# Kernel tuning notes

Hardware: AMD Instinct MI355X
Metric: run time of the kernel (lower is better)

Reference implementation:

```python
import jax, jax.numpy as jnp
import numpy as np

# Dimensions: D must equal C_CHUNK**2 (original code's view+transpose requires it)
D = 4096        # flattened input dim per sample
C_CHUNK = 64    # chunk_size (rows of G per chunk)
N_CHUNKS = D // C_CHUNK  # = 64
H = 512         # hidden dim of forward_func MLP
C_OUT = 8       # output classes of forward_func
B = 8           # batch size (state_batch has 2*B rows)
EPS_G = 1e-4    # metric regularizer (constant under grad)


def setup_inputs() -> dict:
    key = jax.random.key(0)
    ks = jax.random.split(key, 6)
    t = jax.random.uniform(ks[0], (1,), dtype=jnp.float32)
    state_batch = jax.random.normal(ks[1], (2 * B, D), dtype=jnp.float32)
    x0_batch = jax.random.normal(ks[2], (B, D), dtype=jnp.float32)
    x1_batch = jax.random.normal(ks[3], (B, D), dtype=jnp.float32)
    W1 = jax.random.normal(ks[4], (D, H), dtype=jnp.float32) / np.float32(np.sqrt(D))
    W2 = jax.random.normal(ks[5], (H, C_OUT), dtype=jnp.float32) / np.float32(np.sqrt(H))
    return {"t": t, "state_batch": state_batch, "x0_batch": x0_batch,
            "x1_batch": x1_batch, "W1": W1, "W2": W2}


def _accel_per_sample(x, v, W1, W2):
    """Chunked Christoffel-symbol contraction for one sample.
    x: [D] current point, v: [D] deviation velocity. Returns a: [D]."""
    def f(xi):  # forward_func: 2-layer tanh MLP, [D] -> [C_OUT]
        return jnp.tanh(xi @ W1) @ W2

    ones = jnp.ones((D,), x.dtype)

    def chunk_sums(xi):
        # G = J^T J + eps*I; row_sums[i] = sum_j G[i,j] computed without
        # materializing the D x D metric: J^T (J @ 1)  (+ const eps on diag).
        J = jax.jacrev(f)(xi)              # [C_OUT, D]
        row = J.T @ (J @ ones)             # [D]
        return row.reshape(N_CHUNKS, C_CHUNK).sum(axis=1)  # [N_CHUNKS]

    g = jax.jacrev(chunk_sums)(x)          # [N_CHUNKS, D] = dG_chunk_sum/dx
    g = g.reshape(N_CHUNKS, C_CHUNK, C_CHUNK)
    g = g / (jnp.linalg.norm(g, axis=2, keepdims=True) + 1e-6)
    Gamma = 0.5 * (g + jnp.swapaxes(g, 1, 2))   # symmetrized [nc, c, c]
    vc = v.reshape(N_CHUNKS, C_CHUNK)
    # a_chunk[i] = -sum_k Gamma[i,k] v_i v_k  (Christoffel quadratic in v)
    a = -jnp.einsum('nik,ni,nk->ni', Gamma, vc, vc)
    return a.reshape(D)


def reference(t, state_batch, x0_batch, x1_batch, W1, W2):
    ts = t[0]
    Bn = state_batch.shape[0] // 2
    deviation = state_batch[:Bn]
    dev_velocity = state_batch[Bn:]
    window = 4.0 * ts * (1.0 - ts)
    x = x0_batch + ts * (x1_batch - x0_batch) + window * deviation  # [B, D]
    a = jax.vmap(_accel_per_sample, in_axes=(0, 0, None, None))(x, dev_velocity, W1, W2)
    a = a / (jnp.linalg.norm(dev_velocity, axis=1, keepdims=True) + 1e-6)
    restoration = -0.1 * deviation
    return jnp.concatenate([dev_velocity, a + restoration], axis=0)  # [2B, D]
```

## Files before the change

### kernel.cpp

```cpp
#include <hip/hip_runtime.h>

#define D 4096
#define H 512
#define NCH 64
#define CCH 64
#define B 8
#define COUT 8

typedef __bf16 bf16x8 __attribute__((ext_vector_type(8)));
typedef float  f32x4  __attribute__((ext_vector_type(4)));

#define OFF_P    0
#define OFF_UP   (OFF_P + NCH*H)
#define OFF_S    (OFF_UP + NCH*B*H)
#define OFF_ST2  (OFF_S + B*H)
#define OFF_Q    (OFF_ST2 + B*H)
#define OFF_C    (OFF_Q + B*H)
#define OFF_VN   (OFF_C + H)
#define OFF_A1   (OFF_VN + 64)
#define OFF_ZB   (OFF_A1 + B*NCH*CCH)
#define OFF_W1H  (OFF_ZB + B*64*4096)
#define OFF_W1L  (OFF_W1H + (D*H)/2)
#define OFF_WH   (OFF_W1L + (D*H)/2)
#define OFF_WL   (OFF_WH + (B*NCH*H)/2)

__device__ __forceinline__ unsigned short f2bf(float x) {
    unsigned int u = __float_as_uint(x);
    unsigned int r = (u + 0x7FFFu + ((u >> 16) & 1u)) >> 16;
    return (unsigned short)r;
}
__device__ __forceinline__ float bf2f(unsigned short s) {
    return __uint_as_float(((unsigned int)s) << 16);
}

__global__ void k1_reduce_w1(const float* __restrict__ W1,
                             const float* __restrict__ state,
                             const float* __restrict__ x0,
                             const float* __restrict__ x1,
                             const float* __restrict__ tptr,
                             float* __restrict__ ws) {
    int n   = blockIdx.x;
    int ht  = blockIdx.y;
    int tid = threadIdx.x;
    int h   = ht * 128 + tid;

    __shared__ float xs[B][64];
    float ts = tptr[0];
    float window = 4.f * ts * (1.f - ts);
    if (tid < 64) {
        int d = n * 64 + tid;
        for (int b = 0; b < B; ++b) {
            float a0 = x0[b * D + d];
            float a1v = x1[b * D + d];
            float dev = state[b * D + d];
            xs[b][tid] = a0 + ts * (a1v - a0) + window * dev;
        }
    }
    __syncthreads();

    unsigned short* __restrict__ W1Hp = (unsigned short*)(ws + OFF_W1H);
    unsigned short* __restrict__ W1Lp = (unsigned short*)(ws + OFF_W1L);

    float p = 0.f;
    float up[B];
#pragma unroll
    for (int b = 0; b < B; ++b) up[b] = 0.f;
    for (int j = 0; j < 64; ++j) {
        int d = n * 64 + j;
        float wv = W1[(size_t)d * H + h];
        unsigned short hi = f2bf(wv);
        W1Hp[d * H + h] = hi;
        W1Lp[d * H + h] = f2bf(wv - bf2f(hi));
        p += wv;
#pragma unroll
        for (int b = 0; b < B; ++b) up[b] += wv * xs[b][j];
    }
    ws[OFF_P + n * H + h] = p;
    for (int b = 0; b < B; ++b) ws[OFF_UP + (n * B + b) * H + h] = up[b];
}

__global__ void k2_sample(const float* __restrict__ W2,
                          const float* __restrict__ state,
                          float* __restrict__ ws) {
    int b = blockIdx.x, tid = threadIdx.x;
    int wid = tid >> 6, lane = tid & 63;
    __shared__ float lm[8][8];
    __shared__ float ms[8];
    __shared__ float lv[8];

    int h = tid;
    float u = 0.f, c = 0.f;
    for (int n = 0; n < NCH; ++n) {
        u += ws[OFF_UP + (n * B + b) * H + h];
        c += ws[OFF_P + n * H + h];
    }
    float tt  = tanhf(u);
    float s   = 1.f - tt * tt;
    float st2 = -2.f * tt * s;
    ws[OFF_S   + b * H + h] = s;
    ws[OFF_ST2 + b * H + h] = st2;
    ws[OFF_C   + h] = c;

    const float4* w2p = (const float4*)(W2 + h * 8);
    float4 w2a = w2p[0], w2b = w2p[1];
    float w2r[8] = {w2a.x, w2a.y, w2a.z, w2a.w, w2b.x, w2b.y, w2b.z, w2b.w};

    float cs = c * s;
    float pr[8];
#pragma unroll
    for (int o = 0; o < 8; ++o) pr[o] = cs * w2r[o];
#pragma unroll
    for (int mk = 1; mk < 64; mk <<= 1)
#pragma unroll
        for (int o = 0; o < 8; ++o) pr[o] += __shfl_xor(pr[o], mk);
    if (lane == 0)
#pragma unroll
        for (int o = 0; o < 8; ++o) lm[wid][o] = pr[o];

    float v2 = 0.f;
    const float* v = state + (size_t)(B + b) * D;
    for (int j = 0; j < D / H; ++j) { float vv = v[j * H + h]; v2 += vv * vv; }
#pragma unroll
    for (int mk = 1; mk < 64; mk <<= 1) v2 += __shfl_xor(v2, mk);
    if (lane == 0) lv[wid] = v2;
    __syncthreads();

    if (tid < 8) {
        float a = 0.f;
        for (int w = 0; w < 8; ++w) a += lm[w][tid];
        ms[tid] = a;
    }
    if (tid == 0) {
        float a = 0.f;
        for (int w = 0; w < 8; ++w) a += lv[w];
        ws[OFF_VN + b] = sqrtf(a) + 1e-6f;
    }
    __syncthreads();

    float q = 0.f;
#pragma unroll
    for (int o = 0; o < 8; ++o) q += w2r[o] * ms[o];
    ws[OFF_Q + b * H + h] = q;
}

__global__ void k3_w(const float* __restrict__ W2,
                     float* __restrict__ ws) {
    int n = blockIdx.x, b = blockIdx.y, lane = threadIdx.x;
    float M[8];
#pragma unroll
    for (int o = 0; o < 8; ++o) M[o] = 0.f;
    for (int j = 0; j < 8; ++j) {
        int h = j * 64 + lane;
        float ps = ws[OFF_P + n * H + h] * ws[OFF_S + b * H + h];
        const float4* wp = (const float4*)(W2 + h * 8);
        float4 wa = wp[0], wb = wp[1];
        M[0] += ps * wa.x; M[1] += ps * wa.y; M[2] += ps * wa.z; M[3] += ps * wa.w;
        M[4] += ps * wb.x; M[5] += ps * wb.y; M[6] += ps * wb.z; M[7] += ps * wb.w;
    }
#pragma unroll
    for (int mk = 1; mk < 64; mk <<= 1)
#pragma unroll
        for (int o = 0; o < 8; ++o) M[o] += __shfl_xor(M[o], mk);

    unsigned short* __restrict__ WHp = (unsigned short*)(ws + OFF_WH);
    unsigned short* __restrict__ WLp = (unsigned short*)(ws + OFF_WL);
    for (int j = 0; j < 8; ++j) {
        int h = j * 64 + lane;
        const float4* wp = (const float4*)(W2 + h * 8);
        float4 wa = wp[0], wb = wp[1];
        float r = wa.x*M[0] + wa.y*M[1] + wa.z*M[2] + wa.w*M[3]
                + wb.x*M[4] + wb.y*M[5] + wb.z*M[6] + wb.w*M[7];
        float P = ws[OFF_P + n * H + h];
        float wv = ws[OFF_ST2 + b * H + h] * (P * ws[OFF_Q + b * H + h] + ws[OFF_C + h] * r);
        unsigned short hi = f2bf(wv);
        WHp[(b * NCH + n) * H + h] = hi;
        WLp[(b * NCH + n) * H + h] = f2bf(wv - bf2f(hi));
    }
}

__global__ __launch_bounds__(256) void k4_mfma(const float* __restrict__ state,
                                               float* __restrict__ ws) {
    int i   = blockIdx.x;
    int b   = blockIdx.y;
    int tid = threadIdx.x;
    int wid = tid >> 6, lane = tid & 63;
    int r16 = lane & 15;
    int kgrp = (lane >> 4) * 8;

    __shared__ float vsp[64][65];
    __shared__ float gp[2][64][67];
    __shared__ float coefs[64];

    const float* v = state + (size_t)(B + b) * D;
    for (int r = 0; r < 4; ++r) {
        int fidx = tid + r * 256;
        float4 val = ((const float4*)v)[fidx];
        int base = fidx * 4, row = base >> 6, col = base & 63;
        vsp[row][col] = val.x; vsp[row][col+1] = val.y;
        vsp[row][col+2] = val.z; vsp[row][col+3] = val.w;
    }

    const unsigned short* __restrict__ W1Hp = (const unsigned short*)(ws + OFF_W1H);
    const unsigned short* __restrict__ W1Lp = (const unsigned short*)(ws + OFF_W1L);
    const unsigned short* __restrict__ WHp  = (const unsigned short*)(ws + OFF_WH);
    const unsigned short* __restrict__ WLp  = (const unsigned short*)(ws + OFF_WL);

    f32x4 acc[4][4];
    f32x4 z4 = {0.f, 0.f, 0.f, 0.f};
#pragma unroll
    for (int m = 0; m < 4; ++m)
#pragma unroll
        for (int c = 0; c < 4; ++c) acc[m][c] = z4;

    int kb = wid * 128 + kgrp;
#pragma unroll
    for (int ks = 0; ks < 4; ++ks) {
        int k = kb + ks * 32;
        bf16x8 ah[4], al[4], bh[4], bl[4];
#pragma unroll
        for (int m = 0; m < 4; ++m) {
            int off = (b * 64 + m * 16 + r16) * H + k;
            ah[m] = *(const bf16x8*)(WHp + off);
            al[m] = *(const bf16x8*)(WLp + off);
        }
#pragma unroll
        for (int c = 0; c < 4; ++c) {
            int off = (i * 64 + c * 16 + r16) * H + k;
            bh[c] = *(const bf16x8*)(W1Hp + off);
            bl[c] = *(const bf16x8*)(W1Lp + off);
        }
#pragma unroll
        for (int m = 0; m < 4; ++m)
#pragma unroll
            for (int c = 0; c < 4; ++c) {
                acc[m][c] = __builtin_amdgcn_mfma_f32_16x16x32_bf16(ah[m], bh[c], acc[m][c], 0, 0, 0);
                acc[m][c] = __builtin_amdgcn_mfma_f32_16x16x32_bf16(ah[m], bl[c], acc[m][c], 0, 0, 0);
                acc[m][c] = __builtin_amdgcn_mfma_f32_16x16x32_bf16(al[m], bh[c], acc[m][c], 0, 0, 0);
            }
    }

    int rowb = (lane >> 4) * 4;
    if (wid < 2) {
        float (*g)[67] = gp[wid];
#pragma unroll
        for (int m = 0; m < 4; ++m)
#pragma unroll
            for (int c = 0; c < 4; ++c)
#pragma unroll
                for (int e = 0; e < 4; ++e)
                    g[m * 16 + rowb + e][c * 16 + r16] = acc[m][c][e];
    }
    __syncthreads();
    if (wid >= 2) {
        float (*g)[67] = gp[wid - 2];
#pragma unroll
        for (int m = 0; m < 4; ++m)
#pragma unroll
            for (int c = 0; c < 4; ++c)
#pragma unroll
                for (int e = 0; e < 4; ++e)
                    g[m * 16 + rowb + e][c * 16 + r16] += acc[m][c][e];
    }
    __syncthreads();

    if (tid < 64) {
        int n = tid;
        float ss = 0.f, y = 0.f;
        for (int k = 0; k < 64; ++k) {
            float g = gp[0][n][k] + gp[1][n][k];
            ss += g * g;
            y  += g * vsp[n][k];
        }
        float nrm = sqrtf(ss) + 1e-6f;
        ws[OFF_A1 + (size_t)(b * NCH + n) * CCH + i] = y / nrm;
        coefs[n] = vsp[n][i] / nrm;
    }
    __syncthreads();

    float* zb = ws + OFF_ZB + ((size_t)b * 64 + i) * 4096;
    for (int r = 0; r < 16; ++r) {
        int idx = tid + r * 256;
        int n = idx >> 6, k = idx & 63;
        zb[idx] = (gp[0][n][k] + gp[1][n][k]) * coefs[n];
    }
}

__global__ void k5_final(const float* __restrict__ state,
                         const float* __restrict__ ws,
                         float* __restrict__ out) {
    int idx = blockIdx.x * 256 + threadIdx.x;
    float vel = state[32768 + idx];
    out[idx] = vel;
    int b = idx >> 12, e = idx & 4095;
    const float* zb = ws + OFF_ZB + (size_t)b * 64 * 4096 + e;
    float z = 0.f;
    for (int i = 0; i < 64; ++i) z += zb[(size_t)i * 4096];
    float a1 = ws[OFF_A1 + (size_t)b * 4096 + e];
    float av = -0.5f * vel * (a1 + z) / ws[OFF_VN + b];
    out[32768 + idx] = av - 0.1f * state[idx];
}

extern "C" void kernel_launch(void* const* d_in, const int* in_sizes, int n_in,
                              void* d_out, int out_size, void* d_ws, size_t ws_size,
                              hipStream_t stream) {
    const float* t   = (const float*)d_in[0];
    const float* st  = (const float*)d_in[1];
    const float* x0  = (const float*)d_in[2];
    const float* x1  = (const float*)d_in[3];
    const float* W1  = (const float*)d_in[4];
    const float* W2  = (const float*)d_in[5];
    float* out = (float*)d_out;
    float* ws  = (float*)d_ws;

    hipLaunchKernelGGL(k1_reduce_w1, dim3(64, 4), dim3(128), 0, stream, W1, st, x0, x1, t, ws);
    hipLaunchKernelGGL(k2_sample,    dim3(8),     dim3(512), 0, stream, W2, st, ws);
    hipLaunchKernelGGL(k3_w,         dim3(64, 8), dim3(64),  0, stream, W2, ws);
    hipLaunchKernelGGL(k4_mfma,      dim3(64, 8), dim3(256), 0, stream, st, ws);
    hipLaunchKernelGGL(k5_final,     dim3(128),   dim3(256), 0, stream, st, ws, out);
}
```

Before: 117.7 us.

## Vectorize W1 reduction with split-j threads and transposed partial layout

k1 now uses 256 threads, each loading float4 of W1 over an 8-row slice of the chunk, then reduces the partials through shared memory and writes P and UP in an n-contiguous transposed layout. k2 reads those transposed partials with contiguous float4 loads instead of strided scalar loads. k4 drops the shared-memory staging of v and reads v directly from global memory in the epilogue, and several loops get unroll pragmas. The aim is more memory parallelism and wider loads in the W1 pass, at the cost of an extra shared-memory reduction step and scattered transposed stores.

Result: slower. 121.8 us (+3.4%).

```diff
diff --git a/kernel.cpp b/kernel.cpp
--- a/kernel.cpp
+++ b/kernel.cpp
@@ -11,8 +11,9 @@
 typedef float  f32x4  __attribute__((ext_vector_type(4)));
 
 #define OFF_P    0
-#define OFF_UP   (OFF_P + NCH*H)
-#define OFF_S    (OFF_UP + NCH*B*H)
+#define OFF_PHN  (OFF_P + NCH*H)
+#define OFF_UPT  (OFF_PHN + H*NCH)
+#define OFF_S    (OFF_UPT + B*H*NCH)
 #define OFF_ST2  (OFF_S + B*H)
 #define OFF_Q    (OFF_ST2 + B*H)
 #define OFF_C    (OFF_Q + B*H)
@@ -33,18 +34,21 @@
     return __uint_as_float(((unsigned int)s) << 16);
 }
 
-__global__ void k1_reduce_w1(const float* __restrict__ W1,
-                             const float* __restrict__ state,
-                             const float* __restrict__ x0,
-                             const float* __restrict__ x1,
-                             const float* __restrict__ tptr,
-                             float* __restrict__ ws) {
+__global__ __launch_bounds__(256) void k1_reduce_w1(const float* __restrict__ W1,
+                                                    const float* __restrict__ state,
+                                                    const float* __restrict__ x0,
+                                                    const float* __restrict__ x1,
+                                                    const float* __restrict__ tptr,
+                                                    float* __restrict__ ws) {
     int n   = blockIdx.x;
     int ht  = blockIdx.y;
     int tid = threadIdx.x;
-    int h   = ht * 128 + tid;
+    int hq  = ht * 32 + (tid & 31);
+    int jh  = tid >> 5;
 
     __shared__ float xs[B][64];
+    __shared__ f32x4 red[8][32][9];
+
     float ts = tptr[0];
     float window = 4.f * ts * (1.f - ts);
     if (tid < 64) {
@@ -61,22 +65,52 @@
     unsigned short* __restrict__ W1Hp = (unsigned short*)(ws + OFF_W1H);
     unsigned short* __restrict__ W1Lp = (unsigned short*)(ws + OFF_W1L);
 
-    float p = 0.f;
-    float up[B];
-#pragma unroll
-    for (int b = 0; b < B; ++b) up[b] = 0.f;
-    for (int j = 0; j < 64; ++j) {
+    f32x4 p4 = {0.f, 0.f, 0.f, 0.f};
+    f32x4 up[B];
+#pragma unroll
+    for (int b = 0; b < B; ++b) up[b] = p4;
+
+#pragma unroll
+    for (int jj = 0; jj < 8; ++jj) {
+        int j = jh * 8 + jj;
         int d = n * 64 + j;
-        float wv = W1[(size_t)d * H + h];
-        unsigned short hi = f2bf(wv);
-        W1Hp[d * H + h] = hi;
-        W1Lp[d * H + h] = f2bf(wv - bf2f(hi));
-        p += wv;
-#pragma unroll
-        for (int b = 0; b < B; ++b) up[b] += wv * xs[b][j];
-    }
-    ws[OFF_P + n * H + h] = p;
-    for (int b = 0; b < B; ++b) ws[OFF_UP + (n * B + b) * H + h] = up[b];
+        f32x4 w = ((const f32x4*)W1)[d * (H / 4) + hq];
+        p4 += w;
+#pragma unroll
+        for (int b = 0; b < B; ++b) up[b] += w * xs[b][j];
+        unsigned short h0 = f2bf(w.x), h1 = f2bf(w.y), h2 = f2bf(w.z), h3 = f2bf(w.w);
+        ushort4 hv = {h0, h1, h2, h3};
+        ushort4 lv = {f2bf(w.x - bf2f(h0)), f2bf(w.y - bf2f(h1)),
+                      f2bf(w.z - bf2f(h2)), f2bf(w.w - bf2f(h3))};
+        *(ushort4*)(W1Hp + d * H + hq * 4) = hv;
+        *(ushort4*)(W1Lp + d * H + hq * 4) = lv;
+    }
+
+    int l = tid & 31;
+    red[jh][l][0] = p4;
+#pragma unroll
+    for (int b = 0; b < B; ++b) red[jh][l][1 + b] = up[b];
+    __syncthreads();
+
+    if (jh == 0) {
+        f32x4 pt = red[0][l][0];
+        f32x4 ut[B];
+#pragma unroll
+        for (int b = 0; b < B; ++b) ut[b] = red[0][l][1 + b];
+        for (int g = 1; g < 8; ++g) {
+            pt += red[g][l][0];
+#pragma unroll
+            for (int b = 0; b < B; ++b) ut[b] += red[g][l][1 + b];
+        }
+        *(f32x4*)(ws + OFF_P + n * H + hq * 4) = pt;
+#pragma unroll
+        for (int e = 0; e < 4; ++e) ws[OFF_PHN + (hq * 4 + e) * NCH + n] = pt[e];
+#pragma unroll
+        for (int b = 0; b < B; ++b)
+#pragma unroll
+            for (int e = 0; e < 4; ++e)
+                ws[OFF_UPT + (b * H + hq * 4 + e) * NCH + n] = ut[b][e];
+    }
 }
 
 __global__ void k2_sample(const float* __restrict__ W2,
@@ -89,11 +123,14 @@
     __shared__ float lv[8];
 
     int h = tid;
-    float u = 0.f, c = 0.f;
-    for (int n = 0; n < NCH; ++n) {
-        u += ws[OFF_UP + (n * B + b) * H + h];
-        c += ws[OFF_P + n * H + h];
-    }
+    f32x4 u4 = {0.f, 0.f, 0.f, 0.f}, c4 = u4;
+    const f32x4* upp = (const f32x4*)(ws + OFF_UPT + (b * H + h) * NCH);
+    const f32x4* pp  = (const f32x4*)(ws + OFF_PHN + h * NCH);
+#pragma unroll
+    for (int j = 0; j < 16; ++j) { u4 += upp[j]; c4 += pp[j]; }
+    float u = u4.x + u4.y + u4.z + u4.w;
+    float c = c4.x + c4.y + c4.z + c4.w;
+
     float tt  = tanhf(u);
     float s   = 1.f - tt * tt;
     float st2 = -2.f * tt * s;
@@ -119,6 +156,7 @@
 
     float v2 = 0.f;
     const float* v = state + (size_t)(B + b) * D;
+#pragma unroll
     for (int j = 0; j < D / H; ++j) { float vv = v[j * H + h]; v2 += vv * vv; }
 #pragma unroll
     for (int mk = 1; mk < 64; mk <<= 1) v2 += __shfl_xor(v2, mk);
@@ -187,18 +225,8 @@
     int r16 = lane & 15;
     int kgrp = (lane >> 4) * 8;
 
-    __shared__ float vsp[64][65];
     __shared__ float gp[2][64][67];
     __shared__ float coefs[64];
-
-    const float* v = state + (size_t)(B + b) * D;
-    for (int r = 0; r < 4; ++r) {
-        int fidx = tid + r * 256;
-        float4 val = ((const float4*)v)[fidx];
-        int base = fidx * 4, row = base >> 6, col = base & 63;
-        vsp[row][col] = val.x; vsp[row][col+1] = val.y;
-        vsp[row][col+2] = val.z; vsp[row][col+3] = val.w;
-    }
 
     const unsigned short* __restrict__ W1Hp = (const unsigned short*)(ws + OFF_W1H);
     const unsigned short* __restrict__ W1Lp = (const unsigned short*)(ws + OFF_W1L);
@@ -263,21 +291,25 @@
     }
     __syncthreads();
 
+    const float* v = state + (size_t)(B + b) * D;
+
     if (tid < 64) {
         int n = tid;
         float ss = 0.f, y = 0.f;
+#pragma unroll 8
         for (int k = 0; k < 64; ++k) {
             float g = gp[0][n][k] + gp[1][n][k];
             ss += g * g;
-            y  += g * vsp[n][k];
+            y  += g * v[n * 64 + k];
         }
         float nrm = sqrtf(ss) + 1e-6f;
         ws[OFF_A1 + (size_t)(b * NCH + n) * CCH + i] = y / nrm;
-        coefs[n] = vsp[n][i] / nrm;
+        coefs[n] = v[n * 64 + i] / nrm;
     }
     __syncthreads();
 
     float* zb = ws + OFF_ZB + ((size_t)b * 64 + i) * 4096;
+#pragma unroll
     for (int r = 0; r < 16; ++r) {
         int idx = tid + r * 256;
         int n = idx >> 6, k = idx & 63;
@@ -294,6 +326,7 @@
     int b = idx >> 12, e = idx & 4095;
     const float* zb = ws + OFF_ZB + (size_t)b * 64 * 4096 + e;
     float z = 0.f;
+#pragma unroll 8
     for (int i = 0; i < 64; ++i) z += zb[(size_t)i * 4096];
     float a1 = ws[OFF_A1 + (size_t)b * 4096 + e];
     float av = -0.5f * vel * (a1 + z) / ws[OFF_VN + b];
@@ -312,7 +345,7 @@
     float* out = (float*)d_out;
     float* ws  = (float*)d_ws;
 
-    hipLaunchKernelGGL(k1_reduce_w1, dim3(64, 4), dim3(128), 0, stream, W1, st, x0, x1, t, ws);
+    hipLaunchKernelGGL(k1_reduce_w1, dim3(64, 4), dim3(256), 0, stream, W1, st, x0, x1, t, ws);
     hipLaunchKernelGGL(k2_sample,    dim3(8),     dim3(512), 0, stream, W2, st, ws);
     hipLaunchKernelGGL(k3_w,         dim3(64, 8), dim3(64),  0, stream, W2, ws);
     hipLaunchKernelGGL(k4_mfma,      dim3(64, 8), dim3(256), 0, stream, st, ws);
```
